# Performance work log

Measured on AMD Instinct MI355X. Metric: run time of the kernel, lower is better.

Reference implementation:

```python
import jax, jax.numpy as jnp
import numpy as np

B, LQ, LK = 8, 64, 256
E, H, D, NH = 128, 4, 32, 128  # embed_time, num_heads, input_dim, nhidden
EK = E // H


def setup_inputs() -> dict:
    key = jax.random.key(0)
    ks = jax.random.split(key, 10)
    s = 1.0 / np.sqrt(E)
    so = 1.0 / np.sqrt(D * H)
    return {
        "query": jax.random.normal(ks[0], (B, LQ, E), jnp.float32),
        "key": jax.random.normal(ks[1], (B, LK, E), jnp.float32),
        "value": jax.random.normal(ks[2], (B, LK, D), jnp.float32),
        "mask": jax.random.randint(ks[3], (B, LK, D), 0, 2, jnp.int32),
        "Wq": jax.random.uniform(ks[4], (E, E), jnp.float32, -s, s),
        "bq": jax.random.uniform(ks[5], (E,), jnp.float32, -s, s),
        "Wk": jax.random.uniform(ks[6], (E, E), jnp.float32, -s, s),
        "bk": jax.random.uniform(ks[7], (E,), jnp.float32, -s, s),
        "Wo": jax.random.uniform(ks[8], (D * H, NH), jnp.float32, -so, so),
        "bo": jax.random.uniform(ks[9], (NH,), jnp.float32, -so, so),
    }


def reference(query, key, value, mask, Wq, bq, Wk, bk, Wo, bo):
    # project and split heads: [B, L, E] -> [B, H, L, EK]
    q = (query @ Wq + bq).reshape(B, LQ, H, EK).transpose(0, 2, 1, 3)
    k = (key @ Wk + bk).reshape(B, LK, H, EK).transpose(0, 2, 1, 3)
    # scores: [B, H, LQ, LK]
    scores = jnp.einsum("bhqe,bhke->bhqk", q, k) / jnp.sqrt(jnp.asarray(EK, q.dtype))
    # per-feature masked logits: [B, H, LQ, LK, D] (broadcast, matches repeat_interleave)
    m = mask[:, None, None, :, :]  # [B,1,1,LK,D]
    logits = jnp.where(m == 0, jnp.asarray(-1e9, q.dtype), scores[..., None])
    p = jax.nn.softmax(logits, axis=-2)  # softmax over LK, per feature channel
    # weighted sum over LK: [B, H, LQ, D]
    x = jnp.sum(p * value[:, None, None, :, :], axis=-2)
    # merge heads: [B, LQ, H*D]
    x = x.transpose(0, 2, 1, 3).reshape(B, LQ, H * D)
    return x @ Wo + bo
```

## Files before the change

### kernel.cpp

```cpp
#include <hip/hip_runtime.h>

#define B_ 8
#define LQ_ 64
#define LK_ 256
#define E_ 128
#define H_ 4
#define D_ 32
#define NH_ 128
#define EK_ 32


#define RAW_BARRIER() asm volatile("s_waitcnt lgkmcnt(0)\n\ts_barrier" ::: "memory")

__global__ __launch_bounds__(512, 2) void fused_attn_kernel(
    const float* __restrict__ query, const float* __restrict__ key,
    const float* __restrict__ value, const int* __restrict__ mask,
    const float* __restrict__ Wq, const float* __restrict__ bq,
    const float* __restrict__ Wk,
    const float* __restrict__ Wo, const float* __restrict__ bo,
    float* __restrict__ out)
{
    const int blk0 = blockIdx.x;
    const int blk  = (blk0 & 7) * 32 + (blk0 >> 3);
    const int b  = blk >> 5;
    const int q0 = (blk & 31) * 2;
    const int t  = threadIdx.x;

    extern __shared__ float dyn[];
    float* qrow  = dyn;
    float* qpart = dyn + 256;
    float* qp    = dyn + 1280;
    float* g     = dyn + 1536;
    float* kt    = dyn + 2560;
    float* spart = dyn + 2560;
    float* e_lds = dyn + 10752;
    float* nump  = dyn + 12800;
    float* denp  = dyn + 16896;
    float* x     = dyn + 20992;
    float* opart = dyn + 21248;

    float4 qv0;
    if (t < 64)
        qv0 = reinterpret_cast<const float4*>(
            query + ((size_t)(b * LQ_) + q0) * E_)[t];

    const int col2  = t & 127;
    const int slab2 = t >> 7;
    float wqr[32];
    {
        const float* wqp = Wq + (size_t)(slab2 * 32) * E_ + col2;
        #pragma unroll
        for (int j = 0; j < 32; ++j) wqr[j] = wqp[(size_t)j * E_];
    }

    const int e4 = t >> 2, p4 = t & 3;
    float4 wkr[8];
    {
        const float4* wk4 =
            reinterpret_cast<const float4*>(Wk + (size_t)e4 * E_ + p4 * EK_);
        #pragma unroll
        for (int j = 0; j < 8; ++j) wkr[j] = wk4[j];
    }

    {
        const float4* kb4 =
            reinterpret_cast<const float4*>(key + (size_t)b * LK_ * E_);
        #pragma unroll
        for (int i = 0; i < 16; ++i) {
            const int slot = i * 512 + t;
            const int k = slot >> 5;
            const int p = slot & 31;
            const float4* src = kb4 + (k * 32 + (p ^ (k & 7)));
            __builtin_amdgcn_global_load_lds(
                (const __attribute__((address_space(1))) void*)src,
                (__attribute__((address_space(3))) void*)(&kt[slot * 4]),
                16, 0, 0);
        }
    }

    const int d  = t & 31;
    const int kg = t >> 5;
    float vv[16], mfv[16];
    {
        const float* vb = value + ((size_t)(b * LK_) + kg * 16) * D_ + d;
        const int*   mb = mask  + ((size_t)(b * LK_) + kg * 16) * D_ + d;
        #pragma unroll
        for (int j = 0; j < 16; ++j) {
            vv[j]  = vb[j * D_];
            mfv[j] = (float)mb[j * D_];
        }
    }

    float wor[32];
    {
        const float* wop = Wo + (size_t)(slab2 * 32) * NH_ + col2;
        #pragma unroll
        for (int j = 0; j < 32; ++j) wor[j] = wop[(size_t)j * NH_];
    }

    if (t < 64) {
        reinterpret_cast<float4*>(qrow)[t] = qv0;
    }
    RAW_BARRIER();

    {
        const float4* qr0 = reinterpret_cast<const float4*>(qrow + slab2 * 32);
        const float4* qr1 = reinterpret_cast<const float4*>(qrow + 128 + slab2 * 32);
        float acc0 = 0.0f, acc1 = 0.0f;
        #pragma unroll
        for (int j = 0; j < 8; ++j) {
            float4 q0v = qr0[j];
            float4 q1v = qr1[j];
            const float w0 = wqr[j * 4 + 0];
            const float w1 = wqr[j * 4 + 1];
            const float w2 = wqr[j * 4 + 2];
            const float w3 = wqr[j * 4 + 3];
            acc0 = fmaf(q0v.x, w0, acc0); acc1 = fmaf(q1v.x, w0, acc1);
            acc0 = fmaf(q0v.y, w1, acc0); acc1 = fmaf(q1v.y, w1, acc1);
            acc0 = fmaf(q0v.z, w2, acc0); acc1 = fmaf(q1v.z, w2, acc1);
            acc0 = fmaf(q0v.w, w3, acc0); acc1 = fmaf(q1v.w, w3, acc1);
        }
        qpart[(slab2 * 2 + 0) * 128 + col2] = acc0;
        qpart[(slab2 * 2 + 1) * 128 + col2] = acc1;
    }
    RAW_BARRIER();

    if (t < 256) {
        const int col = t & 127, r = t >> 7;
        float s = bq[col];
        #pragma unroll
        for (int slab = 0; slab < 4; ++slab)
            s += qpart[(slab * 2 + r) * 128 + col];
        qp[r * 128 + col] = s;
    }
    RAW_BARRIER();

    {
        const float inv_sqrt_ek = 0.17677669529663687f;
        #pragma unroll
        for (int r = 0; r < 2; ++r) {
            const float4* qp4 = reinterpret_cast<const float4*>(qp + r * 128 + p4 * EK_);
            float acc = 0.0f;
            #pragma unroll
            for (int j = 0; j < 8; ++j) {
                float4 pv = qp4[j];
                acc = fmaf(wkr[j].x, pv.x, acc);
                acc = fmaf(wkr[j].y, pv.y, acc);
                acc = fmaf(wkr[j].z, pv.z, acc);
                acc = fmaf(wkr[j].w, pv.w, acc);
            }
            g[(r * 4 + p4) * 128 + e4] = acc * inv_sqrt_ek;
        }
    }
    __syncthreads();

    const int k5  = t & 127;
    const int eq5 = t >> 7;
    float acc0[8] = {0.f, 0.f, 0.f, 0.f, 0.f, 0.f, 0.f, 0.f};
    float acc1[8] = {0.f, 0.f, 0.f, 0.f, 0.f, 0.f, 0.f, 0.f};
    {
        const int xr = k5 & 7;
        const float4* kt4 = reinterpret_cast<const float4*>(kt);
        const float4* g4  = reinterpret_cast<const float4*>(g);
        #pragma unroll
        for (int j = 0; j < 8; ++j) {
            const int jj = eq5 * 8 + j;
            const float4 kv0 = kt4[k5 * 32 + (jj ^ xr)];
            const float4 kv1 = kt4[(k5 + 128) * 32 + (jj ^ xr)];
            #pragma unroll
            for (int rh = 0; rh < 8; ++rh) {
                const float4 gg = g4[rh * 32 + jj];
                acc0[rh] = fmaf(kv0.x, gg.x, acc0[rh]);
                acc0[rh] = fmaf(kv0.y, gg.y, acc0[rh]);
                acc0[rh] = fmaf(kv0.z, gg.z, acc0[rh]);
                acc0[rh] = fmaf(kv0.w, gg.w, acc0[rh]);
                acc1[rh] = fmaf(kv1.x, gg.x, acc1[rh]);
                acc1[rh] = fmaf(kv1.y, gg.y, acc1[rh]);
                acc1[rh] = fmaf(kv1.z, gg.z, acc1[rh]);
                acc1[rh] = fmaf(kv1.w, gg.w, acc1[rh]);
            }
        }
    }
    __syncthreads();

    #pragma unroll
    for (int rh = 0; rh < 8; ++rh) {
        spart[(eq5 * 8 + rh) * 256 + k5]       = acc0[rh];
        spart[(eq5 * 8 + rh) * 256 + k5 + 128] = acc1[rh];
    }
    __syncthreads();

    {
        const int w = t >> 6;
        const int l = t & 63;
        const float4* sp4 = reinterpret_cast<const float4*>(spart);
        float4 s0 = sp4[w * 64 + l];
        #pragma unroll
        for (int eq = 1; eq < 4; ++eq) {
            float4 s1 = sp4[(eq * 8 + w) * 64 + l];
            s0.x += s1.x; s0.y += s1.y; s0.z += s1.z; s0.w += s1.w;
        }
        float m = fmaxf(fmaxf(s0.x, s0.y), fmaxf(s0.z, s0.w));
        #pragma unroll
        for (int off = 32; off; off >>= 1)
            m = fmaxf(m, __shfl_xor(m, off));
        float4 e;
        e.x = __expf(s0.x - m); e.y = __expf(s0.y - m);
        e.z = __expf(s0.z - m); e.w = __expf(s0.w - m);
        *reinterpret_cast<float4*>(&e_lds[w * LK_ + l * 4]) = e;
    }
    __syncthreads();

    {
        float num[8] = {0.f, 0.f, 0.f, 0.f, 0.f, 0.f, 0.f, 0.f};
        float den[8] = {0.f, 0.f, 0.f, 0.f, 0.f, 0.f, 0.f, 0.f};
        #pragma unroll
        for (int jq = 0; jq < 4; ++jq) {
            const float4 mv4 = make_float4(mfv[jq*4+0]*vv[jq*4+0], mfv[jq*4+1]*vv[jq*4+1],
                                           mfv[jq*4+2]*vv[jq*4+2], mfv[jq*4+3]*vv[jq*4+3]);
            const float4 mf4 = make_float4(mfv[jq*4+0], mfv[jq*4+1],
                                           mfv[jq*4+2], mfv[jq*4+3]);
            #pragma unroll
            for (int rh = 0; rh < 8; ++rh) {
                float4 ev = *reinterpret_cast<const float4*>(
                    &e_lds[rh * LK_ + kg * 16 + jq * 4]);
                num[rh] = fmaf(ev.x, mv4.x, num[rh]);
                num[rh] = fmaf(ev.y, mv4.y, num[rh]);
                num[rh] = fmaf(ev.z, mv4.z, num[rh]);
                num[rh] = fmaf(ev.w, mv4.w, num[rh]);
                den[rh] = fmaf(ev.x, mf4.x, den[rh]);
                den[rh] = fmaf(ev.y, mf4.y, den[rh]);
                den[rh] = fmaf(ev.z, mf4.z, den[rh]);
                den[rh] = fmaf(ev.w, mf4.w, den[rh]);
            }
        }
        #pragma unroll
        for (int rh = 0; rh < 8; ++rh) {
            nump[(kg * 8 + rh) * 32 + d] = num[rh];
            denp[(kg * 8 + rh) * 32 + d] = den[rh];
        }
    }
    __syncthreads();

    if (t < 256) {
        const int rh = t >> 5, dd = t & 31;
        float n = 0.f, dn = 0.f;
        #pragma unroll
        for (int k2 = 0; k2 < 16; ++k2) {
            n  += nump[(k2 * 8 + rh) * 32 + dd];
            dn += denp[(k2 * 8 + rh) * 32 + dd];
        }
        x[(rh >> 2) * 128 + (rh & 3) * 32 + dd] = n / dn;
    }
    __syncthreads();

    {
        const int c0 = slab2 * 32;
        const float4* x40 = reinterpret_cast<const float4*>(x + c0);
        const float4* x41 = reinterpret_cast<const float4*>(x + 128 + c0);
        float acc0o = 0.f, acc1o = 0.f;
        #pragma unroll
        for (int j = 0; j < 8; ++j) {
            float4 xv0 = x40[j];
            float4 xv1 = x41[j];
            const float w0 = wor[j * 4 + 0];
            const float w1 = wor[j * 4 + 1];
            const float w2 = wor[j * 4 + 2];
            const float w3 = wor[j * 4 + 3];
            acc0o = fmaf(xv0.x, w0, acc0o); acc1o = fmaf(xv1.x, w0, acc1o);
            acc0o = fmaf(xv0.y, w1, acc0o); acc1o = fmaf(xv1.y, w1, acc1o);
            acc0o = fmaf(xv0.z, w2, acc0o); acc1o = fmaf(xv1.z, w2, acc1o);
            acc0o = fmaf(xv0.w, w3, acc0o); acc1o = fmaf(xv1.w, w3, acc1o);
        }
        opart[(slab2 * 2 + 0) * 128 + col2] = acc0o;
        opart[(slab2 * 2 + 1) * 128 + col2] = acc1o;
    }
    __syncthreads();

    if (t < 256) {
        const int col = t & 127, r = t >> 7;
        float s = bo[col];
        #pragma unroll
        for (int eq = 0; eq < 4; ++eq)
            s += opart[(eq * 2 + r) * 128 + col];
        out[((size_t)(b * LQ_) + q0 + r) * NH_ + col] = s;
    }
}

extern "C" void kernel_launch(void* const* d_in, const int* in_sizes, int n_in,
                              void* d_out, int out_size, void* d_ws, size_t ws_size,
                              hipStream_t stream) {
    const float* query = (const float*)d_in[0];
    const float* key   = (const float*)d_in[1];
    const float* value = (const float*)d_in[2];
    const int*   mask  = (const int*)d_in[3];
    const float* Wq    = (const float*)d_in[4];
    const float* bq    = (const float*)d_in[5];
    const float* Wk    = (const float*)d_in[6];
    const float* Wo    = (const float*)d_in[8];
    const float* bo    = (const float*)d_in[9];
    float* out = (float*)d_out;

    const size_t lds_bytes = 35328 * sizeof(float);
    static bool attr_set = false;
    if (!attr_set) {
        hipFuncSetAttribute(reinterpret_cast<const void*>(fused_attn_kernel),
                            hipFuncAttributeMaxDynamicSharedMemorySize,
                            (int)lds_bytes);
        attr_set = true;
    }

    fused_attn_kernel<<<B_ * (LQ_ / 2), 512, lds_bytes, stream>>>(
        query, key, value, mask, Wq, bq, Wk, Wo, bo, out);
}
```

Before: 16.16 us.

## Retile score computation to four keys per thread and pre-reduce PV partials via shuffle

The QK score stage now has each thread cover four key rows (64-key stride) over four embedding chunks instead of two keys over eight chunks. Each g load is reused across four key vectors, but there are eight partial slices to sum in the softmax stage instead of four, and the LDS layout is enlarged and shifted to hold them. In the PV stage, adjacent kg partial sums are combined with a cross-lane shuffle before being written to shared memory, which halves the nump/denp writes and the final reduction loop. The tradeoffs are higher register pressure from 32 accumulators and more LDS use per block.

```diff
diff --git a/kernel.cpp b/kernel.cpp
--- a/kernel.cpp
+++ b/kernel.cpp
@@ -33,11 +33,11 @@
     float* g     = dyn + 1536;
     float* kt    = dyn + 2560;
     float* spart = dyn + 2560;
-    float* e_lds = dyn + 10752;
-    float* nump  = dyn + 12800;
-    float* denp  = dyn + 16896;
-    float* x     = dyn + 20992;
-    float* opart = dyn + 21248;
+    float* e_lds = dyn + 18944;
+    float* nump  = dyn + 20992;
+    float* denp  = dyn + 23040;
+    float* x     = dyn + 25088;
+    float* opart = dyn + 25344;
 
     float4 qv0;
     if (t < 64)
@@ -154,30 +154,43 @@
     }
     __syncthreads();
 
-    const int k5  = t & 127;
-    const int eq5 = t >> 7;
-    float acc0[8] = {0.f, 0.f, 0.f, 0.f, 0.f, 0.f, 0.f, 0.f};
-    float acc1[8] = {0.f, 0.f, 0.f, 0.f, 0.f, 0.f, 0.f, 0.f};
+    const int k5  = t & 63;
+    const int eq5 = t >> 6;
+    float a0[8] = {0.f,0.f,0.f,0.f,0.f,0.f,0.f,0.f};
+    float a1[8] = {0.f,0.f,0.f,0.f,0.f,0.f,0.f,0.f};
+    float a2[8] = {0.f,0.f,0.f,0.f,0.f,0.f,0.f,0.f};
+    float a3[8] = {0.f,0.f,0.f,0.f,0.f,0.f,0.f,0.f};
     {
         const int xr = k5 & 7;
         const float4* kt4 = reinterpret_cast<const float4*>(kt);
         const float4* g4  = reinterpret_cast<const float4*>(g);
         #pragma unroll
-        for (int j = 0; j < 8; ++j) {
-            const int jj = eq5 * 8 + j;
-            const float4 kv0 = kt4[k5 * 32 + (jj ^ xr)];
-            const float4 kv1 = kt4[(k5 + 128) * 32 + (jj ^ xr)];
+        for (int j = 0; j < 4; ++j) {
+            const int jj = eq5 * 4 + j;
+            const int js = jj ^ xr;
+            const float4 kv0 = kt4[(k5      ) * 32 + js];
+            const float4 kv1 = kt4[(k5 +  64) * 32 + js];
+            const float4 kv2 = kt4[(k5 + 128) * 32 + js];
+            const float4 kv3 = kt4[(k5 + 192) * 32 + js];
             #pragma unroll
             for (int rh = 0; rh < 8; ++rh) {
                 const float4 gg = g4[rh * 32 + jj];
-                acc0[rh] = fmaf(kv0.x, gg.x, acc0[rh]);
-                acc0[rh] = fmaf(kv0.y, gg.y, acc0[rh]);
-                acc0[rh] = fmaf(kv0.z, gg.z, acc0[rh]);
-                acc0[rh] = fmaf(kv0.w, gg.w, acc0[rh]);
-                acc1[rh] = fmaf(kv1.x, gg.x, acc1[rh]);
-                acc1[rh] = fmaf(kv1.y, gg.y, acc1[rh]);
-                acc1[rh] = fmaf(kv1.z, gg.z, acc1[rh]);
-                acc1[rh] = fmaf(kv1.w, gg.w, acc1[rh]);
+                a0[rh] = fmaf(kv0.x, gg.x, a0[rh]);
+                a0[rh] = fmaf(kv0.y, gg.y, a0[rh]);
+                a0[rh] = fmaf(kv0.z, gg.z, a0[rh]);
+                a0[rh] = fmaf(kv0.w, gg.w, a0[rh]);
+                a1[rh] = fmaf(kv1.x, gg.x, a1[rh]);
+                a1[rh] = fmaf(kv1.y, gg.y, a1[rh]);
+                a1[rh] = fmaf(kv1.z, gg.z, a1[rh]);
+                a1[rh] = fmaf(kv1.w, gg.w, a1[rh]);
+                a2[rh] = fmaf(kv2.x, gg.x, a2[rh]);
+                a2[rh] = fmaf(kv2.y, gg.y, a2[rh]);
+                a2[rh] = fmaf(kv2.z, gg.z, a2[rh]);
+                a2[rh] = fmaf(kv2.w, gg.w, a2[rh]);
+                a3[rh] = fmaf(kv3.x, gg.x, a3[rh]);
+                a3[rh] = fmaf(kv3.y, gg.y, a3[rh]);
+                a3[rh] = fmaf(kv3.z, gg.z, a3[rh]);
+                a3[rh] = fmaf(kv3.w, gg.w, a3[rh]);
             }
         }
     }
@@ -185,8 +198,11 @@
 
     #pragma unroll
     for (int rh = 0; rh < 8; ++rh) {
-        spart[(eq5 * 8 + rh) * 256 + k5]       = acc0[rh];
-        spart[(eq5 * 8 + rh) * 256 + k5 + 128] = acc1[rh];
+        float* sp = &spart[(eq5 * 8 + rh) * 256];
+        sp[k5      ] = a0[rh];
+        sp[k5 +  64] = a1[rh];
+        sp[k5 + 128] = a2[rh];
+        sp[k5 + 192] = a3[rh];
     }
     __syncthreads();
 
@@ -196,8 +212,8 @@
         const float4* sp4 = reinterpret_cast<const float4*>(spart);
         float4 s0 = sp4[w * 64 + l];
         #pragma unroll
-        for (int eq = 1; eq < 4; ++eq) {
-            float4 s1 = sp4[(eq * 8 + w) * 64 + l];
+        for (int ec = 1; ec < 8; ++ec) {
+            float4 s1 = sp4[(ec * 8 + w) * 64 + l];
             s0.x += s1.x; s0.y += s1.y; s0.z += s1.z; s0.w += s1.w;
         }
         float m = fmaxf(fmaxf(s0.x, s0.y), fmaxf(s0.z, s0.w));
@@ -212,8 +228,8 @@
     __syncthreads();
 
     {
-        float num[8] = {0.f, 0.f, 0.f, 0.f, 0.f, 0.f, 0.f, 0.f};
-        float den[8] = {0.f, 0.f, 0.f, 0.f, 0.f, 0.f, 0.f, 0.f};
+        float num[8] = {0.f,0.f,0.f,0.f,0.f,0.f,0.f,0.f};
+        float den[8] = {0.f,0.f,0.f,0.f,0.f,0.f,0.f,0.f};
         #pragma unroll
         for (int jq = 0; jq < 4; ++jq) {
             const float4 mv4 = make_float4(mfv[jq*4+0]*vv[jq*4+0], mfv[jq*4+1]*vv[jq*4+1],
@@ -236,8 +252,16 @@
         }
         #pragma unroll
         for (int rh = 0; rh < 8; ++rh) {
-            nump[(kg * 8 + rh) * 32 + d] = num[rh];
-            denp[(kg * 8 + rh) * 32 + d] = den[rh];
+            num[rh] += __shfl_xor(num[rh], 32);
+            den[rh] += __shfl_xor(den[rh], 32);
+        }
+        if ((kg & 1) == 0) {
+            const int kgp = kg >> 1;
+            #pragma unroll
+            for (int rh = 0; rh < 8; ++rh) {
+                nump[(kgp * 8 + rh) * 32 + d] = num[rh];
+                denp[(kgp * 8 + rh) * 32 + d] = den[rh];
+            }
         }
     }
     __syncthreads();
@@ -246,7 +270,7 @@
         const int rh = t >> 5, dd = t & 31;
         float n = 0.f, dn = 0.f;
         #pragma unroll
-        for (int k2 = 0; k2 < 16; ++k2) {
+        for (int k2 = 0; k2 < 8; ++k2) {
             n  += nump[(k2 * 8 + rh) * 32 + dd];
             dn += denp[(k2 * 8 + rh) * 32 + dd];
         }
```

New measurement: 17.33 us. 1.07x slower.
